# Kernel optimization log

Measured on AMD Instinct MI355X. Metric: run time of the kernel, lower is better.

Reference implementation:

```python
import jax, jax.numpy as jnp
import numpy as np

B, S, T = 256, 1024, 64


def setup_inputs() -> dict:
    key = jax.random.key(0)
    k1, k2, k3 = jax.random.split(key, 3)
    emissions = jax.random.normal(k1, (B, S, T), dtype=jnp.float32)
    tags = jax.random.randint(k2, (B, S), 0, T)
    # xavier_uniform_ init for U [T, T]
    limit = float(np.sqrt(6.0 / (T + T)))
    U = jax.random.uniform(k3, (T, T), dtype=jnp.float32, minval=-limit, maxval=limit)
    b_start = jnp.zeros((T,), dtype=jnp.float32)
    b_end = jnp.zeros((T,), dtype=jnp.float32)
    return {"emissions": emissions, "tags": tags, "U": U, "b_start": b_start, "b_end": b_end}


def reference(emissions, tags, U, b_start, b_end):
    # boundary energies (mask=None path): add b_start at t=0, b_end at t=S-1
    x = emissions.at[:, 0, :].add(b_start).at[:, -1, :].add(b_end)

    # --- path energy of gold tags ---
    # emission energy: gather x at gold tags, sum over time -> [B]
    emis_e = jnp.take_along_axis(x, tags[..., None], axis=-1)[..., 0].sum(axis=1)
    # transition energy: U[tags_t, tags_{t+1}] summed over time -> [B]
    trans_e = U[tags[:, :-1], tags[:, 1:]].sum(axis=1)
    path_e = emis_e + trans_e

    # --- free energy (log partition) via forward algorithm scan ---
    def step(alpha, xt):
        # alpha [B,T] prev scores; xt [B,T] emissions at t
        # next_score[b, i, j] = alpha[b,i] + U[i,j] + xt[b,j]
        next_a = alpha[:, :, None] + U[None, :, :] + xt[:, None, :]
        return jax.nn.logsumexp(next_a, axis=1), None

    alpha0 = x[:, 0, :]                       # [B,T]
    xs = jnp.moveaxis(x[:, 1:, :], 1, 0)      # [S-1, B, T]
    alpha, _ = jax.lax.scan(step, alpha0, xs)
    free_e = jax.nn.logsumexp(alpha, axis=1)  # [B]

    nll = -path_e + free_e
    return jnp.mean(nll)
```

## Files before the change

### kernel.cpp

```cpp
#include <hip/hip_runtime.h>
#include <hip/hip_bf16.h>

constexpr int B = 256, S = 1024, T = 64;
constexpr float LOG2E = 1.4426950408889634f;
constexpr float LN2   = 0.6931471805599453f;

typedef _Float16 h2 __attribute__((ext_vector_type(2)));

static __device__ __forceinline__ float dot2f(unsigned int abits, h2 b, float c) {
    return __builtin_amdgcn_fdot2(__builtin_bit_cast(h2, abits), b, c, false);
}
static __device__ __forceinline__ unsigned int pack2(float lo, float hi) {
    return __builtin_bit_cast(unsigned int, __builtin_amdgcn_cvt_pkrtz(lo, hi));
}

__global__ __launch_bounds__(64, 1) void crf_pair(
        const float* __restrict__ emis, const int* __restrict__ tags,
        const float* __restrict__ U,    const float* __restrict__ bs,
        const float* __restrict__ be,   float* __restrict__ nll) {
    __shared__ __align__(16) _Float16 qsh[2][2][T];
    const int chain = blockIdx.x;
    const int j = threadIdx.x;
    const float* eb = emis + (size_t)chain * (S * T);
    const int*   tb = tags + (size_t)chain * S;

    h2 WA[32], WB[32];
#pragma unroll
    for (int m = 0; m < 32; ++m) {
        WA[m] = __builtin_bit_cast(h2, pack2(
            __builtin_amdgcn_exp2f(U[(2 * m)     * T + j] * LOG2E),
            __builtin_amdgcn_exp2f(U[(2 * m + 1) * T + j] * LOG2E)));
        WB[m] = __builtin_bit_cast(h2, pack2(
            __builtin_amdgcn_exp2f(U[j * T + 2 * m]     * LOG2E),
            __builtin_amdgcn_exp2f(U[j * T + 2 * m + 1] * LOG2E)));
    }

    float pe = 0.f;
#pragma unroll
    for (int sc = 0; sc < 16; ++sc) {
        int s  = sc * 64 + j;
        int tg = tb[s];
        float e = eb[(size_t)s * T + tg];
        if (s == 0)     e += bs[tg];
        if (s == S - 1) e += be[tg];
        pe += e;
        if (s < S - 1)  pe += U[tg * T + tb[s + 1]];
    }
#pragma unroll
    for (int m = 1; m < 64; m <<= 1) pe += __shfl_xor(pe, m, 64);

    float aA = (eb[j] + bs[j]) * LOG2E;
    float MA = aA;
#pragma unroll
    for (int m = 1; m < 64; m <<= 1) MA = fmaxf(MA, __shfl_xor(MA, m, 64));
    float pA = __builtin_amdgcn_exp2f(aA - MA);
    int ciA = 0; const float cfA = MA;

    float aB = (eb[(size_t)(S - 1) * T + j] + be[j]) * LOG2E;
    float MB = aB;
#pragma unroll
    for (int m = 1; m < 64; m <<= 1) MB = fmaxf(MB, __shfl_xor(MB, m, 64));
    float pB = __builtin_amdgcn_exp2f(aB - MB);
    int ciB = 0; const float cfB = MB;

    auto renormA = [&](float ss) -> float {
        unsigned int sb = __builtin_amdgcn_readfirstlane(__float_as_uint(ss));
        int e = (int)((sb >> 23) & 0xFF);
        ciA += e - 127;
        return ss * __uint_as_float((unsigned int)(254 - e) << 23);
    };
    auto renormB = [&](float ss) -> float {
        unsigned int sb = __builtin_amdgcn_readfirstlane(__float_as_uint(ss));
        int e = (int)((sb >> 23) & 0xFF);
        ciB += e - 127;
        return ss * __uint_as_float((unsigned int)(254 - e) << 23);
    };

    auto dstep = [&](float xA, float xB, int par) {
        float exA = __builtin_amdgcn_exp2f(xA * LOG2E);
        float exB = __builtin_amdgcn_exp2f(xB * LOG2E);
        qsh[par][0][j] = (_Float16)pA;
        qsh[par][1][j] = (_Float16)pB;
        const uint4* qa = (const uint4*)qsh[par][0];
        const uint4* qb = (const uint4*)qsh[par][1];
        float a0 = 0.f, a1 = 0.f, a2 = 0.f, a3 = 0.f;
        float b0 = 0.f, b1 = 0.f, b2 = 0.f, b3 = 0.f;
#pragma unroll
        for (int g = 0; g < 8; ++g) {
            uint4 va = qa[g], vb = qb[g];
            a0 = dot2f(va.x, WA[4 * g + 0], a0);
            a1 = dot2f(va.y, WA[4 * g + 1], a1);
            a2 = dot2f(va.z, WA[4 * g + 2], a2);
            a3 = dot2f(va.w, WA[4 * g + 3], a3);
            b0 = dot2f(vb.x, WB[4 * g + 0], b0);
            b1 = dot2f(vb.y, WB[4 * g + 1], b1);
            b2 = dot2f(vb.z, WB[4 * g + 2], b2);
            b3 = dot2f(vb.w, WB[4 * g + 3], b3);
        }
        pA = renormA((a0 + a1) + (a2 + a3)) * exA;
        pB = renormB((b0 + b1) + (b2 + b3)) * exB;
    };
    auto fstep = [&](float xA, int par) {
        float exA = __builtin_amdgcn_exp2f(xA * LOG2E);
        qsh[par][0][j] = (_Float16)pA;
        const uint4* qa = (const uint4*)qsh[par][0];
        float a0 = 0.f, a1 = 0.f, a2 = 0.f, a3 = 0.f;
#pragma unroll
        for (int g = 0; g < 8; ++g) {
            uint4 va = qa[g];
            a0 = dot2f(va.x, WA[4 * g + 0], a0);
            a1 = dot2f(va.y, WA[4 * g + 1], a1);
            a2 = dot2f(va.z, WA[4 * g + 2], a2);
            a3 = dot2f(va.w, WA[4 * g + 3], a3);
        }
        pA = renormA((a0 + a1) + (a2 + a3)) * exA;
    };

    auto xldA = [&](int u) {
        int uu = u < 510 ? u : 510;
        float v = eb[(size_t)(1 + uu) * T + j];
        return u < 511 ? v : 0.0f;
    };
    auto xldB = [&](int u) {
        int uu = u < 510 ? u : 510;
        return eb[(size_t)(1022 - uu) * T + j];
    };

    float xaA[8], xbA[8], xaB[8], xbB[8];
#pragma unroll
    for (int u = 0; u < 8; ++u) { xaA[u] = xldA(u); xaB[u] = xldB(u); }
    int u0 = 0;
    for (int k = 0; k < 31; ++k) {
#pragma unroll
        for (int v = 0; v < 8; ++v) { xbA[v] = xldA(u0 + 8 + v); xbB[v] = xldB(u0 + 8 + v); }
#pragma unroll
        for (int v = 0; v < 8; ++v) dstep(xaA[v], xaB[v], v & 1);
#pragma unroll
        for (int v = 0; v < 8; ++v) { xaA[v] = xldA(u0 + 16 + v); xaB[v] = xldB(u0 + 16 + v); }
#pragma unroll
        for (int v = 0; v < 8; ++v) dstep(xbA[v], xbB[v], v & 1);
        u0 += 16;
    }
#pragma unroll
    for (int v = 0; v < 8; ++v) { xbA[v] = xldA(504 + v); xbB[v] = xldB(504 + v); }
#pragma unroll
    for (int v = 0; v < 8; ++v) dstep(xaA[v], xaB[v], v & 1);
#pragma unroll
    for (int v = 0; v < 7; ++v) dstep(xbA[v], xbB[v], v & 1);
    fstep(xbA[7], 1);

    float v = pA * pB;
#pragma unroll
    for (int m = 1; m < 64; m <<= 1) v += __shfl_xor(v, m, 64);
    if (j == 0) {
        float free_e = LN2 * (__builtin_amdgcn_logf(v)
                              + cfA + (float)ciA + cfB + (float)ciB);
        nll[chain] = free_e - pe;
    }
}

__global__ __launch_bounds__(256, 1) void crf_reduce(const float* __restrict__ nll,
                                                     float* __restrict__ out) {
    float v = nll[threadIdx.x];
#pragma unroll
    for (int m = 1; m < 64; m <<= 1) v += __shfl_xor(v, m, 64);
    __shared__ float acc[4];
    if ((threadIdx.x & 63) == 0) acc[threadIdx.x >> 6] = v;
    __syncthreads();
    if (threadIdx.x == 0) out[0] = (acc[0] + acc[1] + acc[2] + acc[3]) * (1.0f / B);
}

extern "C" void kernel_launch(void* const* d_in, const int* in_sizes, int n_in,
                              void* d_out, int out_size, void* d_ws, size_t ws_size,
                              hipStream_t stream) {
    const float* emis = (const float*)d_in[0];
    const int*   tags = (const int*)d_in[1];
    const float* U    = (const float*)d_in[2];
    const float* bs   = (const float*)d_in[3];
    const float* be   = (const float*)d_in[4];
    float* nll = (float*)d_ws;

    crf_pair<<<dim3(B), dim3(64), 0, stream>>>(emis, tags, U, bs, be, nll);
    crf_reduce<<<dim3(1), dim3(256), 0, stream>>>(nll, (float*)d_out);
}
```

Before: 192.5 us.

## Replace LDS broadcast with readlane and packed half FMA for both chains

The forward and backward alpha vectors are packed into one half2 register, and each step broadcasts lane values with readlane instead of a round trip through shared memory. Both chains are then updated by one packed fp16 FMA per source tag, using a weight array that interleaves the forward and backward transitions. This removes the LDS write/read and the dot2 reductions from the serial critical path. In exchange it issues 64 readlanes per step and accumulates in fp16 rather than fp32, which reduces accuracy and risks overflow or precision loss.

```diff
diff --git a/kernel.cpp b/kernel.cpp
--- a/kernel.cpp
+++ b/kernel.cpp
@@ -7,32 +7,28 @@
 
 typedef _Float16 h2 __attribute__((ext_vector_type(2)));
 
-static __device__ __forceinline__ float dot2f(unsigned int abits, h2 b, float c) {
-    return __builtin_amdgcn_fdot2(__builtin_bit_cast(h2, abits), b, c, false);
+static __device__ __forceinline__ h2 pk(float lo, float hi) {
+    return __builtin_bit_cast(h2, __builtin_amdgcn_cvt_pkrtz(lo, hi));
 }
-static __device__ __forceinline__ unsigned int pack2(float lo, float hi) {
-    return __builtin_bit_cast(unsigned int, __builtin_amdgcn_cvt_pkrtz(lo, hi));
+static __device__ __forceinline__ h2 bcast(unsigned int bits, int lane) {
+    return __builtin_bit_cast(h2, __builtin_amdgcn_readlane(bits, lane));
 }
 
 __global__ __launch_bounds__(64, 1) void crf_pair(
         const float* __restrict__ emis, const int* __restrict__ tags,
         const float* __restrict__ U,    const float* __restrict__ bs,
         const float* __restrict__ be,   float* __restrict__ nll) {
-    __shared__ __align__(16) _Float16 qsh[2][2][T];
     const int chain = blockIdx.x;
     const int j = threadIdx.x;
     const float* eb = emis + (size_t)chain * (S * T);
     const int*   tb = tags + (size_t)chain * S;
 
-    h2 WA[32], WB[32];
+    h2 Wpk[64];
 #pragma unroll
-    for (int m = 0; m < 32; ++m) {
-        WA[m] = __builtin_bit_cast(h2, pack2(
-            __builtin_amdgcn_exp2f(U[(2 * m)     * T + j] * LOG2E),
-            __builtin_amdgcn_exp2f(U[(2 * m + 1) * T + j] * LOG2E)));
-        WB[m] = __builtin_bit_cast(h2, pack2(
-            __builtin_amdgcn_exp2f(U[j * T + 2 * m]     * LOG2E),
-            __builtin_amdgcn_exp2f(U[j * T + 2 * m + 1] * LOG2E)));
+    for (int i = 0; i < 64; ++i) {
+        float wf = __builtin_amdgcn_exp2f(U[i * T + j] * LOG2E);
+        float wb = __builtin_amdgcn_exp2f(U[j * T + i] * LOG2E);
+        Wpk[i] = pk(wf, wb);
     }
 
     float pe = 0.f;
@@ -63,57 +59,30 @@
     float pB = __builtin_amdgcn_exp2f(aB - MB);
     int ciB = 0; const float cfB = MB;
 
-    auto renormA = [&](float ss) -> float {
-        unsigned int sb = __builtin_amdgcn_readfirstlane(__float_as_uint(ss));
-        int e = (int)((sb >> 23) & 0xFF);
-        ciA += e - 127;
-        return ss * __uint_as_float((unsigned int)(254 - e) << 23);
-    };
-    auto renormB = [&](float ss) -> float {
-        unsigned int sb = __builtin_amdgcn_readfirstlane(__float_as_uint(ss));
-        int e = (int)((sb >> 23) & 0xFF);
-        ciB += e - 127;
-        return ss * __uint_as_float((unsigned int)(254 - e) << 23);
-    };
+    h2 ppk = pk(pA, pB);
 
-    auto dstep = [&](float xA, float xB, int par) {
+    auto dstep = [&](float xA, float xB) {
         float exA = __builtin_amdgcn_exp2f(xA * LOG2E);
         float exB = __builtin_amdgcn_exp2f(xB * LOG2E);
-        qsh[par][0][j] = (_Float16)pA;
-        qsh[par][1][j] = (_Float16)pB;
-        const uint4* qa = (const uint4*)qsh[par][0];
-        const uint4* qb = (const uint4*)qsh[par][1];
-        float a0 = 0.f, a1 = 0.f, a2 = 0.f, a3 = 0.f;
-        float b0 = 0.f, b1 = 0.f, b2 = 0.f, b3 = 0.f;
+        unsigned int qb = __builtin_bit_cast(unsigned int, ppk);
+        h2 a0 = {0, 0}, a1 = {0, 0}, a2 = {0, 0}, a3 = {0, 0};
 #pragma unroll
-        for (int g = 0; g < 8; ++g) {
-            uint4 va = qa[g], vb = qb[g];
-            a0 = dot2f(va.x, WA[4 * g + 0], a0);
-            a1 = dot2f(va.y, WA[4 * g + 1], a1);
-            a2 = dot2f(va.z, WA[4 * g + 2], a2);
-            a3 = dot2f(va.w, WA[4 * g + 3], a3);
-            b0 = dot2f(vb.x, WB[4 * g + 0], b0);
-            b1 = dot2f(vb.y, WB[4 * g + 1], b1);
-            b2 = dot2f(vb.z, WB[4 * g + 2], b2);
-            b3 = dot2f(vb.w, WB[4 * g + 3], b3);
+        for (int i = 0; i < 64; i += 4) {
+            a0 = __builtin_elementwise_fma(bcast(qb, i + 0), Wpk[i + 0], a0);
+            a1 = __builtin_elementwise_fma(bcast(qb, i + 1), Wpk[i + 1], a1);
+            a2 = __builtin_elementwise_fma(bcast(qb, i + 2), Wpk[i + 2], a2);
+            a3 = __builtin_elementwise_fma(bcast(qb, i + 3), Wpk[i + 3], a3);
         }
-        pA = renormA((a0 + a1) + (a2 + a3)) * exA;
-        pB = renormB((b0 + b1) + (b2 + b3)) * exB;
-    };
-    auto fstep = [&](float xA, int par) {
-        float exA = __builtin_amdgcn_exp2f(xA * LOG2E);
-        qsh[par][0][j] = (_Float16)pA;
-        const uint4* qa = (const uint4*)qsh[par][0];
-        float a0 = 0.f, a1 = 0.f, a2 = 0.f, a3 = 0.f;
-#pragma unroll
-        for (int g = 0; g < 8; ++g) {
-            uint4 va = qa[g];
-            a0 = dot2f(va.x, WA[4 * g + 0], a0);
-            a1 = dot2f(va.y, WA[4 * g + 1], a1);
-            a2 = dot2f(va.z, WA[4 * g + 2], a2);
-            a3 = dot2f(va.w, WA[4 * g + 3], a3);
-        }
-        pA = renormA((a0 + a1) + (a2 + a3)) * exA;
+        h2 s2 = (a0 + a1) + (a2 + a3);
+        float ssA = (float)s2[0];
+        float ssB = (float)s2[1];
+        unsigned int bA = __builtin_amdgcn_readfirstlane(__float_as_uint(ssA));
+        int eA = (int)((bA >> 23) & 0xFF); ciA += eA - 127;
+        float scA = __uint_as_float((unsigned int)(254 - eA) << 23);
+        unsigned int bB = __builtin_amdgcn_readfirstlane(__float_as_uint(ssB));
+        int eB = (int)((bB >> 23) & 0xFF); ciB += eB - 127;
+        float scB = __uint_as_float((unsigned int)(254 - eB) << 23);
+        ppk = pk(ssA * scA * exA, ssB * scB * exB);
     };
 
     auto xldA = [&](int u) {
@@ -134,27 +103,30 @@
 #pragma unroll
         for (int v = 0; v < 8; ++v) { xbA[v] = xldA(u0 + 8 + v); xbB[v] = xldB(u0 + 8 + v); }
 #pragma unroll
-        for (int v = 0; v < 8; ++v) dstep(xaA[v], xaB[v], v & 1);
+        for (int v = 0; v < 8; ++v) dstep(xaA[v], xaB[v]);
 #pragma unroll
         for (int v = 0; v < 8; ++v) { xaA[v] = xldA(u0 + 16 + v); xaB[v] = xldB(u0 + 16 + v); }
 #pragma unroll
-        for (int v = 0; v < 8; ++v) dstep(xbA[v], xbB[v], v & 1);
+        for (int v = 0; v < 8; ++v) dstep(xbA[v], xbB[v]);
         u0 += 16;
     }
 #pragma unroll
     for (int v = 0; v < 8; ++v) { xbA[v] = xldA(504 + v); xbB[v] = xldB(504 + v); }
 #pragma unroll
-    for (int v = 0; v < 8; ++v) dstep(xaA[v], xaB[v], v & 1);
+    for (int v = 0; v < 8; ++v) dstep(xaA[v], xaB[v]);
 #pragma unroll
-    for (int v = 0; v < 7; ++v) dstep(xbA[v], xbB[v], v & 1);
-    fstep(xbA[7], 1);
+    for (int v = 0; v < 7; ++v) dstep(xbA[v], xbB[v]);
+    float pBf = (float)ppk[1];
+    float CB  = cfB + (float)ciB;
+    dstep(xbA[7], 0.0f);
+    float pAf = (float)ppk[0];
+    float CA  = cfA + (float)ciA;
 
-    float v = pA * pB;
+    float v = pAf * pBf;
 #pragma unroll
     for (int m = 1; m < 64; m <<= 1) v += __shfl_xor(v, m, 64);
     if (j == 0) {
-        float free_e = LN2 * (__builtin_amdgcn_logf(v)
-                              + cfA + (float)ciA + cfB + (float)ciB);
+        float free_e = LN2 * (__builtin_amdgcn_logf(v) + CA + CB);
         nll[chain] = free_e - pe;
     }
 }
```

Measured after the change: 187.2 us. 1.03x faster.
